# Kernel optimization log

Hardware: AMD Instinct MI355X
Metric: run time of the kernel (lower is better)

The kernel has to match this reference:

```python
import jax, jax.numpy as jnp
import numpy as np

N, C_IN, C_RED, H, W = 16, 256, 64, 48, 48


def conv1x1(x, w, b):
    # x: [N, Cin, H, W], w: [Cout, Cin], b: [Cout]
    return jnp.einsum('nchw,oc->nohw', x, w) + b[None, :, None, None]


def setup_inputs() -> dict:
    key = jax.random.key(0)
    ks = jax.random.split(key, 10)
    s_in = 1.0 / np.sqrt(C_IN)
    s_red = 1.0 / np.sqrt(C_RED)
    return {
        'feature_maps': jax.random.normal(ks[0], (N, C_IN, H, W), jnp.float32),
        'global_channel_output': jax.random.normal(ks[1], (N, C_IN, H, W), jnp.float32),
        'Wq': jax.random.uniform(ks[2], (C_RED, C_IN), jnp.float32, -s_in, s_in),
        'bq': jax.random.uniform(ks[3], (C_RED,), jnp.float32, -s_in, s_in),
        'Wk': jax.random.uniform(ks[4], (C_RED, C_IN), jnp.float32, -s_in, s_in),
        'bk': jax.random.uniform(ks[5], (C_RED,), jnp.float32, -s_in, s_in),
        'Wv': jax.random.uniform(ks[6], (C_RED, C_IN), jnp.float32, -s_in, s_in),
        'bv': jax.random.uniform(ks[7], (C_RED,), jnp.float32, -s_in, s_in),
        'Watt': jax.random.uniform(ks[8], (C_IN, C_RED), jnp.float32, -s_red, s_red),
        'batt': jax.random.uniform(ks[9], (C_IN,), jnp.float32, -s_red, s_red),
    }


def reference(feature_maps, global_channel_output, Wq, bq, Wk, bk, Wv, bv, Watt, batt):
    n, _, h, w = feature_maps.shape
    hw = h * w
    q = conv1x1(feature_maps, Wq, bq).reshape(n, -1, hw)   # [N, Cr, HW]
    k = conv1x1(feature_maps, Wk, bk).reshape(n, -1, hw)   # [N, Cr, HW]
    v = conv1x1(feature_maps, Wv, bv).reshape(n, -1, hw)   # [N, Cr, HW]
    # key^T @ query -> [N, HW, HW]
    qk = jnp.einsum('nci,ncj->nij', k, q)
    # global (flattened) softmax over the whole HWxHW matrix per batch element
    qk = jax.nn.softmax(qk.reshape(n, hw * hw), axis=-1).reshape(n, hw, hw)
    att = jnp.einsum('nci,nij->ncj', v, qk).reshape(n, -1, h, w)  # [N, Cr, H, W]
    att = conv1x1(att, Watt, batt)                                 # [N, Cin, H, W]
    return global_channel_output * att + global_channel_output
```

## Files before the change

kernel.cpp:

```cpp
#include <hip/hip_runtime.h>
#include <hip/hip_bf16.h>
#include <stdint.h>

#define NB   16
#define CIN  256
#define CRED 64
#define HW   2304
#define NJT  36
#define NIG  2
#define NIT  18

typedef __bf16 bf16;
typedef __bf16 bf16x8 __attribute__((ext_vector_type(8)));
typedef __bf16 bf16x4 __attribute__((ext_vector_type(4)));
typedef float  f32x4  __attribute__((ext_vector_type(4)));

__global__ __launch_bounds__(256) void prep_kernel(
    const float* __restrict__ Wq, const float* __restrict__ bq,
    const float* __restrict__ Wk, const float* __restrict__ Wv,
    const float* __restrict__ Watt,
    bf16* __restrict__ Wqb, bf16* __restrict__ Wkb, bf16* __restrict__ Wvb,
    bf16* __restrict__ Wab, float* __restrict__ bqs)
{
    const float INVLN2 = 1.44269504088896f;
    int i = blockIdx.x * 256 + threadIdx.x;
    Wqb[i] = (bf16)(Wq[i] * INVLN2);
    Wkb[i] = (bf16)Wk[i];
    Wvb[i] = (bf16)Wv[i];
    Wab[i] = (bf16)Watt[i];
    if (i < CRED) bqs[i] = bq[i] * INVLN2;
}

__global__ __launch_bounds__(256) void qkv_kernel(
    const float* __restrict__ x,
    const bf16* __restrict__ Wqb, const float* __restrict__ bqs,
    const bf16* __restrict__ Wkb, const float* __restrict__ bk,
    const bf16* __restrict__ Wvb, const float* __restrict__ bv,
    bf16* __restrict__ qT, bf16* __restrict__ kT, bf16* __restrict__ v)
{
    __shared__ __align__(16) bf16 sX[32 * 264];
    const int jt = blockIdx.x, n = blockIdx.y;
    const int jbase = jt * 32;
    const int tid = threadIdx.x;
    const int lane = tid & 63, w = tid >> 6;
    const int l15 = lane & 15, q4 = lane >> 4;

    const float* xn = x + ((size_t)n * CIN) * HW + jbase;
    #pragma unroll
    for (int it = 0; it < 8; ++it) {
        int idx = tid + 256 * it;
        int c = idx >> 3, p4 = idx & 7;
        const float4 vv = *(const float4*)(xn + c * HW + p4 * 4);
        sX[(p4 * 4 + 0) * 264 + c] = (bf16)vv.x;
        sX[(p4 * 4 + 1) * 264 + c] = (bf16)vv.y;
        sX[(p4 * 4 + 2) * 264 + c] = (bf16)vv.z;
        sX[(p4 * 4 + 3) * 264 + c] = (bf16)vv.w;
    }
    __syncthreads();

    const bf16*  Ws[3] = {Wqb, Wkb, Wvb};
    const float* bs[3] = {bqs, bk, bv};
    #pragma unroll
    for (int wi = 0; wi < 3; ++wi) {
        bf16x8 a[8];
        const bf16* Wp = Ws[wi] + (w * 16 + l15) * CIN + q4 * 8;
        #pragma unroll
        for (int ks = 0; ks < 8; ++ks) a[ks] = *(const bf16x8*)(Wp + ks * 32);
        f32x4 acc[2] = {};
        #pragma unroll
        for (int nt = 0; nt < 2; ++nt) {
            #pragma unroll
            for (int ks = 0; ks < 8; ++ks) {
                bf16x8 b = *(const bf16x8*)(sX + (nt * 16 + l15) * 264 + ks * 32 + q4 * 8);
                acc[nt] = __builtin_amdgcn_mfma_f32_16x16x32_bf16(a[ks], b, acc[nt], 0, 0, 0);
            }
        }
        const int crb = w * 16 + q4 * 4;
        const float b0 = bs[wi][crb], b1 = bs[wi][crb + 1],
                    b2 = bs[wi][crb + 2], b3 = bs[wi][crb + 3];
        if (wi < 2) {
            bf16* dst = (wi == 0 ? qT : kT) + ((size_t)n * HW) * 64;
            #pragma unroll
            for (int nt = 0; nt < 2; ++nt) {
                int pos = jbase + nt * 16 + l15;
                bf16x4 pk = {(bf16)(acc[nt].x + b0), (bf16)(acc[nt].y + b1),
                             (bf16)(acc[nt].z + b2), (bf16)(acc[nt].w + b3)};
                *(bf16x4*)(dst + pos * 64 + crb) = pk;
            }
        } else {
            bf16* dst = v + ((size_t)n * CRED) * HW;
            #pragma unroll
            for (int nt = 0; nt < 2; ++nt) {
                int pos = jbase + nt * 16 + l15;
                dst[(crb + 0) * HW + pos] = (bf16)(acc[nt].x + b0);
                dst[(crb + 1) * HW + pos] = (bf16)(acc[nt].y + b1);
                dst[(crb + 2) * HW + pos] = (bf16)(acc[nt].z + b2);
                dst[(crb + 3) * HW + pos] = (bf16)(acc[nt].w + b3);
            }
        }
    }
}

__global__ __launch_bounds__(256, 4) void attn_kernel(
    const bf16* __restrict__ qT, const bf16* __restrict__ kT,
    const bf16* __restrict__ v,
    float* __restrict__ OTp, float* __restrict__ Z)
{
    __shared__ __align__(16) bf16 sQP[64 * 72];
    __shared__ __align__(16) bf16 sK[64 * 72];
    __shared__ __align__(16) bf16 sV[64 * 72];
    const int jt = blockIdx.x, ig = blockIdx.y, n = blockIdx.z;
    const int jbase = jt * 64;
    const int tid = threadIdx.x;
    const int lane = tid & 63, w = tid >> 6;
    const int l15 = lane & 15, q4 = lane >> 4;

    {
        const uint4* src = (const uint4*)(qT + ((size_t)n * HW + jbase) * 64);
        uint4* dst = (uint4*)sQP;
        for (int i = tid; i < 512; i += 256) {
            int r = i >> 3, c = i & 7;
            dst[r * 9 + c] = src[r * 8 + c];
        }
    }
    __syncthreads();
    bf16x8 qf[4][2];
    #pragma unroll
    for (int nt = 0; nt < 4; ++nt)
        #pragma unroll
        for (int ks = 0; ks < 2; ++ks)
            qf[nt][ks] = *(const bf16x8*)(sQP + (nt * 16 + l15) * 72 + ks * 32 + q4 * 8);

    f32x4 oacc[4] = {};
    float zacc = 0.f;
    const uint4* ksrc = (const uint4*)(kT + ((size_t)n * HW) * 64);
    const bf16* vbase = v + ((size_t)n * CRED) * HW;

    const int r0 = tid >> 3, c0 = tid & 7;
    const int ibase0 = ig * NIT * 64;

    uint4 kr0 = ksrc[(ibase0 + r0) * 8 + c0];
    uint4 kr1 = ksrc[(ibase0 + r0 + 32) * 8 + c0];
    uint4 vr0 = *(const uint4*)(vbase + (size_t)r0 * HW + ibase0 + c0 * 8);
    uint4 vr1 = *(const uint4*)(vbase + (size_t)(r0 + 32) * HW + ibase0 + c0 * 8);

    uint4* dk = (uint4*)sK;
    uint4* dv = (uint4*)sV;

    for (int it = 0; it < NIT; ++it) {
        const int ibase = ibase0 + it * 64;
        __syncthreads();
        dk[r0 * 9 + c0] = kr0;
        dk[(r0 + 32) * 9 + c0] = kr1;
        dv[r0 * 9 + c0] = vr0;
        dv[(r0 + 32) * 9 + c0] = vr1;
        const int nbase = (it + 1 < NIT) ? ibase + 64 : ibase;
        kr0 = ksrc[(nbase + r0) * 8 + c0];
        kr1 = ksrc[(nbase + r0 + 32) * 8 + c0];
        vr0 = *(const uint4*)(vbase + (size_t)r0 * HW + nbase + c0 * 8);
        vr1 = *(const uint4*)(vbase + (size_t)(r0 + 32) * HW + nbase + c0 * 8);
        __syncthreads();

        bf16x8 kf0 = *(const bf16x8*)(sK + (w * 16 + l15) * 72 + 0 * 32 + q4 * 8);
        bf16x8 kf1 = *(const bf16x8*)(sK + (w * 16 + l15) * 72 + 1 * 32 + q4 * 8);
        #pragma unroll
        for (int nt = 0; nt < 4; ++nt) {
            f32x4 accs = {};
            accs = __builtin_amdgcn_mfma_f32_16x16x32_bf16(kf0, qf[nt][0], accs, 0, 0, 0);
            accs = __builtin_amdgcn_mfma_f32_16x16x32_bf16(kf1, qf[nt][1], accs, 0, 0, 0);
            float p0 = exp2f(accs.x), p1 = exp2f(accs.y);
            float p2 = exp2f(accs.z), p3 = exp2f(accs.w);
            zacc += (p0 + p1) + (p2 + p3);
            bf16x4 pk = {(bf16)p0, (bf16)p1, (bf16)p2, (bf16)p3};
            *(bf16x4*)(sQP + (nt * 16 + l15) * 72 + w * 16 + q4 * 4) = pk;
        }
        __syncthreads();
        bf16x8 vf0 = *(const bf16x8*)(sV + (w * 16 + l15) * 72 + 0 * 32 + q4 * 8);
        bf16x8 vf1 = *(const bf16x8*)(sV + (w * 16 + l15) * 72 + 1 * 32 + q4 * 8);
        #pragma unroll
        for (int nt = 0; nt < 4; ++nt) {
            bf16x8 p0 = *(const bf16x8*)(sQP + (nt * 16 + l15) * 72 + 0 * 32 + q4 * 8);
            bf16x8 p1 = *(const bf16x8*)(sQP + (nt * 16 + l15) * 72 + 1 * 32 + q4 * 8);
            oacc[nt] = __builtin_amdgcn_mfma_f32_16x16x32_bf16(vf0, p0, oacc[nt], 0, 0, 0);
            oacc[nt] = __builtin_amdgcn_mfma_f32_16x16x32_bf16(vf1, p1, oacc[nt], 0, 0, 0);
        }
    }
    float* OTn = OTp + (((size_t)ig * NB + n) * HW) * 64;
    #pragma unroll
    for (int nt = 0; nt < 4; ++nt) {
        int pos = jbase + nt * 16 + l15;
        *(f32x4*)(OTn + pos * 64 + w * 16 + q4 * 4) = oacc[nt];
    }
    #pragma unroll
    for (int off = 32; off > 0; off >>= 1) zacc += __shfl_down(zacc, off);
    if (lane == 0) atomicAdd(Z + n, zacc);
}

__global__ __launch_bounds__(256) void out_kernel(
    const float* __restrict__ OTp, const float* __restrict__ Z,
    const bf16* __restrict__ Wab, const float* __restrict__ batt,
    const float* __restrict__ g, float* __restrict__ out)
{
    __shared__ __align__(16) bf16 sO[64 * 72];
    const int jt = blockIdx.x, n = blockIdx.y;
    const int jbase = jt * 64;
    const int tid = threadIdx.x;
    const int lane = tid & 63, w = tid >> 6;
    const int l15 = lane & 15, q4 = lane >> 4;
    const float invZ = 1.0f / Z[n];

    for (int i = tid; i < 1024; i += 256) {
        int r = i >> 4, c4 = i & 15;
        const float* p = OTp + (((size_t)n * HW) + jbase + r) * 64 + c4 * 4;
        float4 v0 = *(const float4*)(p);
        float4 v1 = *(const float4*)(p + (size_t)NB * HW * 64);
        bf16x4 pk = {(bf16)((v0.x + v1.x) * invZ),
                     (bf16)((v0.y + v1.y) * invZ),
                     (bf16)((v0.z + v1.z) * invZ),
                     (bf16)((v0.w + v1.w) * invZ)};
        *(bf16x4*)(sO + r * 72 + c4 * 4) = pk;
    }
    __syncthreads();

    bf16x8 bfr[4][2];
    #pragma unroll
    for (int nt = 0; nt < 4; ++nt)
        #pragma unroll
        for (int ks = 0; ks < 2; ++ks)
            bfr[nt][ks] = *(const bf16x8*)(sO + (nt * 16 + l15) * 72 + ks * 32 + q4 * 8);

    const float* gp = g + ((size_t)n * CIN) * HW;
    float* op = out + ((size_t)n * CIN) * HW;
    #pragma unroll
    for (int mt = 0; mt < 4; ++mt) {
        const bf16* Wp = Wab + (w * 64 + mt * 16 + l15) * 64 + q4 * 8;
        bf16x8 a0 = *(const bf16x8*)(Wp);
        bf16x8 a1 = *(const bf16x8*)(Wp + 32);
        const int co = w * 64 + mt * 16 + q4 * 4;
        const float c0 = batt[co], c1 = batt[co + 1], c2 = batt[co + 2], c3 = batt[co + 3];
        #pragma unroll
        for (int nt = 0; nt < 4; ++nt) {
            f32x4 acc = {};
            acc = __builtin_amdgcn_mfma_f32_16x16x32_bf16(a0, bfr[nt][0], acc, 0, 0, 0);
            acc = __builtin_amdgcn_mfma_f32_16x16x32_bf16(a1, bfr[nt][1], acc, 0, 0, 0);
            const int pos = jbase + nt * 16 + l15;
            const float g0 = gp[(co + 0) * HW + pos], g1 = gp[(co + 1) * HW + pos];
            const float g2 = gp[(co + 2) * HW + pos], g3 = gp[(co + 3) * HW + pos];
            op[(co + 0) * HW + pos] = g0 * (acc.x + c0 + 1.0f);
            op[(co + 1) * HW + pos] = g1 * (acc.y + c1 + 1.0f);
            op[(co + 2) * HW + pos] = g2 * (acc.z + c2 + 1.0f);
            op[(co + 3) * HW + pos] = g3 * (acc.w + c3 + 1.0f);
        }
    }
}

extern "C" void kernel_launch(void* const* d_in, const int* in_sizes, int n_in,
                              void* d_out, int out_size, void* d_ws, size_t ws_size,
                              hipStream_t stream) {
    const float* x    = (const float*)d_in[0];
    const float* g    = (const float*)d_in[1];
    const float* Wq   = (const float*)d_in[2];
    const float* bq   = (const float*)d_in[3];
    const float* Wk   = (const float*)d_in[4];
    const float* bk   = (const float*)d_in[5];
    const float* Wv   = (const float*)d_in[6];
    const float* bv   = (const float*)d_in[7];
    const float* Watt = (const float*)d_in[8];
    const float* batt = (const float*)d_in[9];
    float* out = (float*)d_out;

    char* ws = (char*)d_ws;
    const size_t qkv_sz = (size_t)NB * HW * CRED * sizeof(bf16);
    bf16*  qT  = (bf16*)(ws);
    bf16*  kT  = (bf16*)(ws + qkv_sz);
    bf16*  vv  = (bf16*)(ws + 2 * qkv_sz);
    float* OTp = (float*)(ws + 3 * qkv_sz);
    char*  w2  = ws + 3 * qkv_sz + (size_t)NIG * NB * HW * CRED * sizeof(float);
    float* Zp  = (float*)(w2);
    bf16*  Wqb = (bf16*)(w2 + 256);
    bf16*  Wkb = Wqb + CRED * CIN;
    bf16*  Wvb = Wkb + CRED * CIN;
    bf16*  Wab = Wvb + CRED * CIN;
    float* bqs = (float*)(Wab + CIN * CRED);

    hipMemsetAsync(Zp, 0, NB * sizeof(float), stream);

    dim3 blk(256);
    prep_kernel<<<dim3(64), blk, 0, stream>>>(Wq, bq, Wk, Wv, Watt, Wqb, Wkb, Wvb, Wab, bqs);
    qkv_kernel<<<dim3(HW / 32, NB), blk, 0, stream>>>(x, Wqb, bqs, Wkb, bk, Wvb, bv, qT, kT, vv);
    attn_kernel<<<dim3(NJT, NIG, NB), blk, 0, stream>>>(qT, kT, vv, OTp, Zp);
    out_kernel<<<dim3(NJT, NB), blk, 0, stream>>>(OTp, Zp, Wab, batt, g, out);
}
```

Measured before the change: 249.2 us.

## Give each wave its own query columns and P buffer in attention

```diff
diff --git a/kernel.cpp b/kernel.cpp
--- a/kernel.cpp
+++ b/kernel.cpp
@@ -6,9 +6,11 @@
 #define CIN  256
 #define CRED 64
 #define HW   2304
-#define NJT  36
-#define NIG  2
-#define NIT  18
+#define NJT_OUT 36
+#define JT_ATT  128
+#define NJT_ATT 18
+#define NIG  4
+#define NIT  9
 
 typedef __bf16 bf16;
 typedef __bf16 bf16x8 __attribute__((ext_vector_type(8)));
@@ -106,32 +108,26 @@
     const bf16* __restrict__ v,
     float* __restrict__ OTp, float* __restrict__ Z)
 {
-    __shared__ __align__(16) bf16 sQP[64 * 72];
     __shared__ __align__(16) bf16 sK[64 * 72];
     __shared__ __align__(16) bf16 sV[64 * 72];
+    __shared__ __align__(16) bf16 sP[128 * 72];
     const int jt = blockIdx.x, ig = blockIdx.y, n = blockIdx.z;
-    const int jbase = jt * 64;
+    const int jbase = jt * JT_ATT;
     const int tid = threadIdx.x;
     const int lane = tid & 63, w = tid >> 6;
     const int l15 = lane & 15, q4 = lane >> 4;
 
+    bf16x8 qf[2][2];
     {
-        const uint4* src = (const uint4*)(qT + ((size_t)n * HW + jbase) * 64);
-        uint4* dst = (uint4*)sQP;
-        for (int i = tid; i < 512; i += 256) {
-            int r = i >> 3, c = i & 7;
-            dst[r * 9 + c] = src[r * 8 + c];
-        }
-    }
-    __syncthreads();
-    bf16x8 qf[4][2];
-    #pragma unroll
-    for (int nt = 0; nt < 4; ++nt)
-        #pragma unroll
-        for (int ks = 0; ks < 2; ++ks)
-            qf[nt][ks] = *(const bf16x8*)(sQP + (nt * 16 + l15) * 72 + ks * 32 + q4 * 8);
-
-    f32x4 oacc[4] = {};
+        const bf16* qn = qT + ((size_t)n * HW + jbase + w * 32) * 64;
+        #pragma unroll
+        for (int nt = 0; nt < 2; ++nt)
+            #pragma unroll
+            for (int ks = 0; ks < 2; ++ks)
+                qf[nt][ks] = *(const bf16x8*)(qn + (nt * 16 + l15) * 64 + ks * 32 + q4 * 8);
+    }
+
+    f32x4 oacc[4][2] = {};
     float zacc = 0.f;
     const uint4* ksrc = (const uint4*)(kT + ((size_t)n * HW) * 64);
     const bf16* vbase = v + ((size_t)n * CRED) * HW;
@@ -146,51 +142,62 @@
 
     uint4* dk = (uint4*)sK;
     uint4* dv = (uint4*)sV;
+    bf16* sPw = sP + (w * 32) * 72;
 
     for (int it = 0; it < NIT; ++it) {
-        const int ibase = ibase0 + it * 64;
         __syncthreads();
         dk[r0 * 9 + c0] = kr0;
         dk[(r0 + 32) * 9 + c0] = kr1;
         dv[r0 * 9 + c0] = vr0;
         dv[(r0 + 32) * 9 + c0] = vr1;
-        const int nbase = (it + 1 < NIT) ? ibase + 64 : ibase;
+        const int nbase = ibase0 + ((it + 1 < NIT) ? (it + 1) * 64 : 0);
         kr0 = ksrc[(nbase + r0) * 8 + c0];
         kr1 = ksrc[(nbase + r0 + 32) * 8 + c0];
         vr0 = *(const uint4*)(vbase + (size_t)r0 * HW + nbase + c0 * 8);
         vr1 = *(const uint4*)(vbase + (size_t)(r0 + 32) * HW + nbase + c0 * 8);
         __syncthreads();
 
-        bf16x8 kf0 = *(const bf16x8*)(sK + (w * 16 + l15) * 72 + 0 * 32 + q4 * 8);
-        bf16x8 kf1 = *(const bf16x8*)(sK + (w * 16 + l15) * 72 + 1 * 32 + q4 * 8);
-        #pragma unroll
-        for (int nt = 0; nt < 4; ++nt) {
-            f32x4 accs = {};
-            accs = __builtin_amdgcn_mfma_f32_16x16x32_bf16(kf0, qf[nt][0], accs, 0, 0, 0);
-            accs = __builtin_amdgcn_mfma_f32_16x16x32_bf16(kf1, qf[nt][1], accs, 0, 0, 0);
-            float p0 = exp2f(accs.x), p1 = exp2f(accs.y);
-            float p2 = exp2f(accs.z), p3 = exp2f(accs.w);
-            zacc += (p0 + p1) + (p2 + p3);
-            bf16x4 pk = {(bf16)p0, (bf16)p1, (bf16)p2, (bf16)p3};
-            *(bf16x4*)(sQP + (nt * 16 + l15) * 72 + w * 16 + q4 * 4) = pk;
-        }
-        __syncthreads();
-        bf16x8 vf0 = *(const bf16x8*)(sV + (w * 16 + l15) * 72 + 0 * 32 + q4 * 8);
-        bf16x8 vf1 = *(const bf16x8*)(sV + (w * 16 + l15) * 72 + 1 * 32 + q4 * 8);
-        #pragma unroll
-        for (int nt = 0; nt < 4; ++nt) {
-            bf16x8 p0 = *(const bf16x8*)(sQP + (nt * 16 + l15) * 72 + 0 * 32 + q4 * 8);
-            bf16x8 p1 = *(const bf16x8*)(sQP + (nt * 16 + l15) * 72 + 1 * 32 + q4 * 8);
-            oacc[nt] = __builtin_amdgcn_mfma_f32_16x16x32_bf16(vf0, p0, oacc[nt], 0, 0, 0);
-            oacc[nt] = __builtin_amdgcn_mfma_f32_16x16x32_bf16(vf1, p1, oacc[nt], 0, 0, 0);
+        #pragma unroll
+        for (int is = 0; is < 4; ++is) {
+            bf16x8 kf0 = *(const bf16x8*)(sK + (is * 16 + l15) * 72 + q4 * 8);
+            bf16x8 kf1 = *(const bf16x8*)(sK + (is * 16 + l15) * 72 + 32 + q4 * 8);
+            #pragma unroll
+            for (int nt = 0; nt < 2; ++nt) {
+                f32x4 accs = {};
+                accs = __builtin_amdgcn_mfma_f32_16x16x32_bf16(kf0, qf[nt][0], accs, 0, 0, 0);
+                accs = __builtin_amdgcn_mfma_f32_16x16x32_bf16(kf1, qf[nt][1], accs, 0, 0, 0);
+                float p0 = exp2f(accs.x), p1 = exp2f(accs.y);
+                float p2 = exp2f(accs.z), p3 = exp2f(accs.w);
+                zacc += (p0 + p1) + (p2 + p3);
+                bf16x4 pk = {(bf16)p0, (bf16)p1, (bf16)p2, (bf16)p3};
+                *(bf16x4*)(sPw + (nt * 16 + l15) * 72 + is * 16 + q4 * 4) = pk;
+            }
+        }
+        bf16x8 pb[2][2];
+        #pragma unroll
+        for (int nt = 0; nt < 2; ++nt) {
+            pb[nt][0] = *(const bf16x8*)(sPw + (nt * 16 + l15) * 72 + q4 * 8);
+            pb[nt][1] = *(const bf16x8*)(sPw + (nt * 16 + l15) * 72 + 32 + q4 * 8);
+        }
+        #pragma unroll
+        for (int ct = 0; ct < 4; ++ct) {
+            bf16x8 vf0 = *(const bf16x8*)(sV + (ct * 16 + l15) * 72 + q4 * 8);
+            bf16x8 vf1 = *(const bf16x8*)(sV + (ct * 16 + l15) * 72 + 32 + q4 * 8);
+            #pragma unroll
+            for (int nt = 0; nt < 2; ++nt) {
+                oacc[ct][nt] = __builtin_amdgcn_mfma_f32_16x16x32_bf16(vf0, pb[nt][0], oacc[ct][nt], 0, 0, 0);
+                oacc[ct][nt] = __builtin_amdgcn_mfma_f32_16x16x32_bf16(vf1, pb[nt][1], oacc[ct][nt], 0, 0, 0);
+            }
         }
     }
     float* OTn = OTp + (((size_t)ig * NB + n) * HW) * 64;
     #pragma unroll
-    for (int nt = 0; nt < 4; ++nt) {
-        int pos = jbase + nt * 16 + l15;
-        *(f32x4*)(OTn + pos * 64 + w * 16 + q4 * 4) = oacc[nt];
-    }
+    for (int ct = 0; ct < 4; ++ct)
+        #pragma unroll
+        for (int nt = 0; nt < 2; ++nt) {
+            int pos = jbase + w * 32 + nt * 16 + l15;
+            *(f32x4*)(OTn + (size_t)pos * 64 + ct * 16 + q4 * 4) = oacc[ct][nt];
+        }
     #pragma unroll
     for (int off = 32; off > 0; off >>= 1) zacc += __shfl_down(zacc, off);
     if (lane == 0) atomicAdd(Z + n, zacc);
@@ -212,12 +219,14 @@
     for (int i = tid; i < 1024; i += 256) {
         int r = i >> 4, c4 = i & 15;
         const float* p = OTp + (((size_t)n * HW) + jbase + r) * 64 + c4 * 4;
-        float4 v0 = *(const float4*)(p);
-        float4 v1 = *(const float4*)(p + (size_t)NB * HW * 64);
-        bf16x4 pk = {(bf16)((v0.x + v1.x) * invZ),
-                     (bf16)((v0.y + v1.y) * invZ),
-                     (bf16)((v0.z + v1.z) * invZ),
-                     (bf16)((v0.w + v1.w) * invZ)};
+        float4 s = *(const float4*)(p);
+        #pragma unroll
+        for (int igx = 1; igx < NIG; ++igx) {
+            float4 t = *(const float4*)(p + (size_t)igx * NB * HW * 64);
+            s.x += t.x; s.y += t.y; s.z += t.z; s.w += t.w;
+        }
+        bf16x4 pk = {(bf16)(s.x * invZ), (bf16)(s.y * invZ),
+                     (bf16)(s.z * invZ), (bf16)(s.w * invZ)};
         *(bf16x4*)(sO + r * 72 + c4 * 4) = pk;
     }
     __syncthreads();
@@ -288,6 +297,6 @@
     dim3 blk(256);
     prep_kernel<<<dim3(64), blk, 0, stream>>>(Wq, bq, Wk, Wv, Watt, Wqb, Wkb, Wvb, Wab, bqs);
     qkv_kernel<<<dim3(HW / 32, NB), blk, 0, stream>>>(x, Wqb, bqs, Wkb, bk, Wvb, bv, qT, kT, vv);
-    attn_kernel<<<dim3(NJT, NIG, NB), blk, 0, stream>>>(qT, kT, vv, OTp, Zp);
-    out_kernel<<<dim3(NJT, NB), blk, 0, stream>>>(OTp, Zp, Wab, batt, g, out);
-}
+    attn_kernel<<<dim3(NJT_ATT, NIG, NB), blk, 0, stream>>>(qT, kT, vv, OTp, Zp);
+    out_kernel<<<dim3(NJT_OUT, NB), blk, 0, stream>>>(OTp, Zp, Wab, batt, g, out);
+}
```

Result: no change. 248.7 us (-0.2%).
